# Kernel optimization log

Measured on AMD Instinct MI355X. Metric: run time of the kernel, lower is better.

Reference implementation:

```python
import jax, jax.numpy as jnp
import numpy as np

C, N, E, G = 8, 50000, 800000, 64
HID, HL, OL = 128, 2, 2
EPS = 1e-5


def sh_l012(vec):
    """e3nn real spherical harmonics l=0,1,2, normalize=True, component normalization. [E,3]->[E,9]"""
    r = jnp.sqrt(jnp.sum(vec * vec, axis=-1, keepdims=True) + 1e-12)
    u = vec / r
    x, y, z = u[:, 0], u[:, 1], u[:, 2]
    s3, s15, s5 = jnp.sqrt(3.0), jnp.sqrt(15.0), jnp.sqrt(5.0)
    y0 = jnp.ones_like(x)[:, None]
    y1 = s3 * u
    y2 = jnp.stack([s15 * x * z, s15 * x * y, s5 * (y * y - 0.5 * (x * x + z * z)),
                    s15 * y * z, 0.5 * s15 * (z * z - x * x)], axis=-1)
    return jnp.concatenate([y0, y1, y2], axis=-1)


def norm_act(s, v, d):
    """e3nn NormActivation(relu, eps): x * relu(n)/n per irrep instance."""
    ns = jnp.sqrt(s * s + EPS * EPS)
    nv = jnp.sqrt(jnp.sum(v * v, -1, keepdims=True) + EPS * EPS)
    nd = jnp.sqrt(jnp.sum(d * d, -1, keepdims=True) + EPS * EPS)
    return s * (jax.nn.relu(ns) / ns), v * (jax.nn.relu(nv) / nv), d * (jax.nn.relu(nd) / nd)


def o3_linear(s, v, d, W0, W1, W2):
    """o3.Linear: mixes multiplicities per l independently."""
    return s @ W0, jnp.einsum('nim,ic->ncm', v, W1), jnp.einsum('nim,ic->ncm', d, W2)


def tf_update(s, v, d, W0, W1, W2, Wd, edge_src, edge_dst):
    """Equivariant transformer update. W0/W1/W2 stacked [3(q,k,v), Cin, C], Wd [3(l), C, C]."""
    qs, qv, qd = norm_act(*o3_linear(s, v, d, W0[0], W1[0], W2[0]))
    ks, kv, kd = norm_act(*o3_linear(s, v, d, W0[1], W1[1], W2[1]))
    vs, vv, vd = norm_act(*o3_linear(s, v, d, W0[2], W1[2], W2[2]))
    # FullyConnectedTensorProduct(q,k)->0e: per-l channel-pair weighted inner products
    logit = (jnp.einsum('ec,ed,cd->e', qs[edge_dst], ks[edge_src], Wd[0])
             + jnp.einsum('ecm,edm,cd->e', qv[edge_dst], kv[edge_src], Wd[1]) / jnp.sqrt(3.0)
             + jnp.einsum('ecm,edm,cd->e', qd[edge_dst], kd[edge_src], Wd[2]) / jnp.sqrt(5.0))
    expv = jnp.exp(logit)
    z = jax.ops.segment_sum(expv, edge_dst, num_segments=N)
    z = jnp.where(z == 0, 1.0, z)
    w = jnp.sqrt(jax.nn.relu(expv / z[edge_dst]))  # relu(alpha).sqrt()
    os = jax.ops.segment_sum(w[:, None] * vs[edge_src], edge_dst, num_segments=N)
    ov = jax.ops.segment_sum(w[:, None, None] * vv[edge_src], edge_dst, num_segments=N)
    od = jax.ops.segment_sum(w[:, None, None] * vd[edge_src], edge_dst, num_segments=N)
    return os, ov, od


def setup_inputs() -> dict:
    key = jax.random.key(0)
    ks = jax.random.split(key, 20)
    inp = {}
    inp['x_scalars'] = jax.random.normal(ks[0], (N, 9), jnp.float32)
    inp['edge_vec'] = jax.random.normal(ks[1], (E, 3), jnp.float32)
    inp['et0_W0'] = jax.random.normal(ks[2], (3, 10, C), jnp.float32) / jnp.sqrt(10.0)
    inp['et0_W1'] = jax.random.normal(ks[3], (3, 1, C), jnp.float32)
    inp['et0_W2'] = jax.random.normal(ks[4], (3, 1, C), jnp.float32)
    inp['et0_Wd'] = jax.random.normal(ks[5], (3, C, C), jnp.float32) / C
    inp['h_W0'] = jax.random.normal(ks[6], (HL, 3, C, C), jnp.float32) / jnp.sqrt(float(C))
    inp['h_W1'] = jax.random.normal(ks[7], (HL, 3, C, C), jnp.float32) / jnp.sqrt(float(C))
    inp['h_W2'] = jax.random.normal(ks[8], (HL, 3, C, C), jnp.float32) / jnp.sqrt(float(C))
    inp['h_Wd'] = jax.random.normal(ks[9], (HL, 3, C, C), jnp.float32) / C
    inp['Wol'] = jax.random.normal(ks[10], (C, HID), jnp.float32) / jnp.sqrt(float(C))
    inp['Wlin'] = jax.random.normal(ks[11], (OL, HID, HID), jnp.float32) / jnp.sqrt(float(HID))
    inp['blin'] = jax.random.normal(ks[12], (OL, HID), jnp.float32) * 0.01
    inp['Wout'] = jax.random.normal(ks[13], (HID, 9), jnp.float32) / jnp.sqrt(float(HID))
    inp['bout'] = jax.random.normal(ks[14], (9,), jnp.float32) * 0.01
    inp['edge_src'] = jax.random.randint(ks[15], (E,), 0, N, jnp.int32)
    inp['edge_dst'] = jax.random.randint(ks[16], (E,), 0, N, jnp.int32)
    inp['batch_seg'] = jnp.sort(jax.random.randint(ks[17], (N,), 0, G, jnp.int32))
    return inp


def reference(x_scalars, edge_vec, et0_W0, et0_W1, et0_W2, et0_Wd,
              h_W0, h_W1, h_W2, h_Wd, Wol, Wlin, blin, Wout, bout,
              edge_src, edge_dst, batch_seg):
    sh = sh_l012(edge_vec)  # [E,9]
    cnt = jnp.maximum(jax.ops.segment_sum(jnp.ones((E,), sh.dtype), edge_dst, num_segments=N), 1.0)
    node_sh = jax.ops.segment_sum(sh, edge_dst, num_segments=N) / cnt[:, None]  # [N,9]
    s = jnp.concatenate([x_scalars, node_sh[:, :1]], axis=1)  # [N,10] 0e
    v = node_sh[:, 1:4][:, None, :]   # [N,1,3] 1e
    d = node_sh[:, 4:9][:, None, :]   # [N,1,5] 2e
    s, v, d = tf_update(s, v, d, et0_W0, et0_W1, et0_W2, et0_Wd, edge_src, edge_dst)
    for l in range(HL):
        hs, hv, hd = tf_update(s, v, d, h_W0[l], h_W1[l], h_W2[l], h_Wd[l], edge_src, edge_dst)
        s, v, d = s + hs, v + hv, d + hd
    # ol: irreps_output -> hidden x 0e (only scalar part maps to scalars)
    h = s @ Wol
    h = h / jnp.maximum(jnp.sqrt(jnp.sum(h * h, 1, keepdims=True)), 1e-12)  # F.normalize
    h = jax.nn.relu(h)
    for i in range(OL):
        h = jax.nn.relu(h @ Wlin[i] + blin[i])
    seg = batch_seg[edge_src]
    cg = jnp.maximum(jax.ops.segment_sum(jnp.ones((E,), h.dtype), seg, num_segments=G), 1.0)
    m = jax.ops.segment_sum(h[edge_src], seg, num_segments=G) / cg[:, None]
    return jax.nn.softmax(m @ Wout + bout, axis=1)
```

## Files before the change

kernel.cpp:

```cpp
#include <hip/hip_runtime.h>
#include <hip/hip_fp16.h>
#include <math.h>

#define NN 50000
#define NE 800000
#define NG 64
#define QH 80
#define KVH 144

__global__ void k_count(const int* __restrict__ esrc, const int* __restrict__ edst,
                        int* __restrict__ indeg_p, int* __restrict__ outdeg_p, int E)
{
  int e = blockIdx.x*blockDim.x + threadIdx.x;
  if (e >= E) return;
  int c = (e & 3) * NN;
  atomicAdd(indeg_p + c + edst[e], 1);
  atomicAdd(outdeg_p + c + esrc[e], 1);
}

__global__ void __launch_bounds__(256) k_scan1(const int* __restrict__ indeg_p,
                                               int* __restrict__ bsum, int N)
{
  __shared__ int sh[256];
  int t = threadIdx.x;
  int lo = blockIdx.x*2048 + t*8;
  int s = 0;
  #pragma unroll
  for (int k = 0; k < 8; ++k) {
    int i = lo + k;
    if (i < N)
      s += indeg_p[i] + indeg_p[NN+i] + indeg_p[2*NN+i] + indeg_p[3*NN+i];
  }
  sh[t] = s;
  __syncthreads();
  for (int off = 128; off > 0; off >>= 1) {
    if (t < off) sh[t] += sh[t+off];
    __syncthreads();
  }
  if (t == 0) bsum[blockIdx.x] = sh[0];
}

__global__ void k_scan2(int* __restrict__ bsum, int nb)
{
  if (threadIdx.x == 0) {
    int run = 0;
    for (int i = 0; i < nb; ++i) { int x = bsum[i]; bsum[i] = run; run += x; }
  }
}

__global__ void __launch_bounds__(256) k_scan3(const int* __restrict__ indeg_p,
                                               const int* __restrict__ outdeg_p,
                                               const int* __restrict__ bsum,
                                               int* __restrict__ rowptr,
                                               int* __restrict__ copybase,
                                               int* __restrict__ outdeg, int N)
{
  __shared__ int sh[256];
  int t = threadIdx.x;
  int lo = blockIdx.x*2048 + t*8;
  int tot[8];
  int s = 0;
  #pragma unroll
  for (int k = 0; k < 8; ++k) {
    int i = lo + k;
    int v = 0;
    if (i < N)
      v = indeg_p[i] + indeg_p[NN+i] + indeg_p[2*NN+i] + indeg_p[3*NN+i];
    tot[k] = v;
    s += v;
  }
  sh[t] = s;
  __syncthreads();
  for (int off = 1; off < 256; off <<= 1) {
    int x = 0;
    if (t >= off) x = sh[t-off];
    __syncthreads();
    if (t >= off) sh[t] += x;
    __syncthreads();
  }
  int run = bsum[blockIdx.x] + (t > 0 ? sh[t-1] : 0);
  #pragma unroll
  for (int k = 0; k < 8; ++k) {
    int i = lo + k;
    if (i < N) {
      int a0 = indeg_p[i], a1 = indeg_p[NN+i], a2 = indeg_p[2*NN+i];
      rowptr[i] = run;
      copybase[i]        = run;
      copybase[NN+i]     = run + a0;
      copybase[2*NN+i]   = run + a0 + a1;
      copybase[3*NN+i]   = run + a0 + a1 + a2;
      outdeg[i] = outdeg_p[i] + outdeg_p[NN+i] + outdeg_p[2*NN+i] + outdeg_p[3*NN+i];
    }
    if (i == N-1) rowptr[N] = run + tot[k];
    run += tot[k];
  }
}

__global__ void k_fill(const int* __restrict__ esrc, const int* __restrict__ edst,
                       const int* __restrict__ copybase, int* __restrict__ cursor_p,
                       int2* __restrict__ csr, int E)
{
  int e = blockIdx.x*blockDim.x + threadIdx.x;
  if (e >= E) return;
  int d = edst[e];
  int c = (e & 3) * NN;
  int slot = copybase[c + d] + atomicAdd(cursor_p + c + d, 1);
  csr[slot] = make_int2(esrc[e], e);
}

template<int CS, int CV, bool INIT>
__global__ void __launch_bounds__(256) k_node_feats(
    const float* __restrict__ in,
    const float* __restrict__ evec,
    const int2* __restrict__ csr,
    const int* __restrict__ rowptr,
    const float* __restrict__ W0,
    const float* __restrict__ W1,
    const float* __restrict__ W2,
    const float* __restrict__ Wd,
    __half* __restrict__ qt,
    __half* __restrict__ kv,
    int N)
{
  int n = blockIdx.x*blockDim.x + threadIdx.x;
  if (n >= N) return;
  float s_in[CS];
  float v_in[CV][3];
  float d_in[CV][5];

  if constexpr (INIT) {
    int b = rowptr[n], e2 = rowptr[n+1];
    float acc[9];
    #pragma unroll
    for (int j = 0; j < 9; ++j) acc[j] = 0.f;
    const float s3  = 1.7320508075688772f;
    const float s15 = 3.872983346207417f;
    const float s5  = 2.23606797749979f;
    for (int s = b; s < e2; ++s) {
      int eid = csr[s].y;
      float vx = evec[3*eid+0], vy = evec[3*eid+1], vz = evec[3*eid+2];
      float r = sqrtf(vx*vx + vy*vy + vz*vz + 1e-12f);
      float x = vx / r, y = vy / r, z = vz / r;
      acc[0] += 1.f;
      acc[1] += s3*x; acc[2] += s3*y; acc[3] += s3*z;
      acc[4] += s15*x*z;
      acc[5] += s15*x*y;
      acc[6] += s5*(y*y - 0.5f*(x*x + z*z));
      acc[7] += s15*y*z;
      acc[8] += 0.5f*s15*(z*z - x*x);
    }
    int dg = e2 - b;
    float inv = 1.f / (float)(dg > 1 ? dg : 1);
    #pragma unroll
    for (int j = 0; j < 9; ++j) s_in[j] = in[(size_t)n*9 + j];
    s_in[9] = acc[0]*inv;
    #pragma unroll
    for (int m = 0; m < 3; ++m) v_in[0][m] = acc[1+m]*inv;
    #pragma unroll
    for (int m = 0; m < 5; ++m) d_in[0][m] = acc[4+m]*inv;
  } else {
    float xf[72];
    const float4* xr = (const float4*)(in + (size_t)n*72);
    #pragma unroll
    for (int k = 0; k < 18; ++k) *(float4*)&xf[k*4] = xr[k];
    #pragma unroll
    for (int i = 0; i < CS; ++i) s_in[i] = xf[i];
    #pragma unroll
    for (int i = 0; i < CV; ++i)
      #pragma unroll
      for (int m = 0; m < 3; ++m) v_in[i][m] = xf[CS + i*3 + m];
    #pragma unroll
    for (int i = 0; i < CV; ++i)
      #pragma unroll
      for (int m = 0; m < 5; ++m) d_in[i][m] = xf[CS + 3*CV + i*5 + m];
  }

  const float inv_s3 = 0.5773502691896258f;
  const float inv_s5 = 0.4472135954999579f;

  #pragma unroll
  for (int t = 0; t < 3; ++t) {
    float ss[8];
    float vv[8][3];
    float dd[8][5];
    #pragma unroll
    for (int c = 0; c < 8; ++c) {
      float a = 0.f;
      #pragma unroll
      for (int i = 0; i < CS; ++i) a += s_in[i]*W0[t*CS*8 + i*8 + c];
      ss[c] = a;
    }
    #pragma unroll
    for (int c = 0; c < 8; ++c)
      #pragma unroll
      for (int m = 0; m < 3; ++m) {
        float a = 0.f;
        #pragma unroll
        for (int i = 0; i < CV; ++i) a += v_in[i][m]*W1[t*CV*8 + i*8 + c];
        vv[c][m] = a;
      }
    #pragma unroll
    for (int c = 0; c < 8; ++c)
      #pragma unroll
      for (int m = 0; m < 5; ++m) {
        float a = 0.f;
        #pragma unroll
        for (int i = 0; i < CV; ++i) a += d_in[i][m]*W2[t*CV*8 + i*8 + c];
        dd[c][m] = a;
      }

    if (t == 0) {
      __half* q = qt + (size_t)n*QH;
      #pragma unroll
      for (int dp = 0; dp < 8; ++dp) {
        float a = 0.f;
        #pragma unroll
        for (int c = 0; c < 8; ++c) a += ss[c]*Wd[0*64 + c*8 + dp];
        q[dp] = __float2half(a);
      }
      #pragma unroll
      for (int dp = 0; dp < 8; ++dp)
        #pragma unroll
        for (int m = 0; m < 3; ++m) {
          float a = 0.f;
          #pragma unroll
          for (int c = 0; c < 8; ++c) a += vv[c][m]*Wd[1*64 + c*8 + dp];
          q[8 + dp*3 + m] = __float2half(a*inv_s3);
        }
      #pragma unroll
      for (int dp = 0; dp < 8; ++dp)
        #pragma unroll
        for (int m = 0; m < 5; ++m) {
          float a = 0.f;
          #pragma unroll
          for (int c = 0; c < 8; ++c) a += dd[c][m]*Wd[2*64 + c*8 + dp];
          q[32 + dp*5 + m] = __float2half(a*inv_s5);
        }
    } else {
      __half* o = kv + (size_t)n*KVH + (t == 1 ? 0 : 72);
      #pragma unroll
      for (int c = 0; c < 8; ++c) o[c] = __float2half(ss[c]);
      #pragma unroll
      for (int c = 0; c < 8; ++c)
        #pragma unroll
        for (int m = 0; m < 3; ++m) o[8 + c*3 + m] = __float2half(vv[c][m]);
      #pragma unroll
      for (int c = 0; c < 8; ++c)
        #pragma unroll
        for (int m = 0; m < 5; ++m) o[32 + c*5 + m] = __float2half(dd[c][m]);
    }
  }
}

#define AT2_NPB 8
__global__ void __launch_bounds__(256) k_attn2(
    const __half* __restrict__ qt,
    const __half* __restrict__ kv,
    const int2* __restrict__ csr,
    const int* __restrict__ rowptr,
    const float* __restrict__ base,
    float* __restrict__ out, int N)
{
  typedef _Float16 h2 __attribute__((ext_vector_type(2)));
  const float LOG2E_HALF = 0.7213475204444817f;

  int t = threadIdx.x;
  int hw = t >> 5, lane = t & 31;
  int n = blockIdx.x*AT2_NPB + hw;
  if (n >= N) return;

  uint4 qraw = make_uint4(0,0,0,0);
  if (lane < 9)
    qraw = *(const uint4*)((const char*)qt + (size_t)n*(QH*2) + (size_t)lane*16);
  h2 qh0 = __builtin_bit_cast(h2, qraw.x);
  h2 qh1 = __builtin_bit_cast(h2, qraw.y);
  h2 qh2 = __builtin_bit_cast(h2, qraw.z);
  h2 qh3 = __builtin_bit_cast(h2, qraw.w);

  int b = rowptr[n], e2 = rowptr[n+1];
  float Z = 0.f;
  float A[8];
  #pragma unroll
  for (int i = 0; i < 8; ++i) A[i] = 0.f;

  const char* kvb = (const char*)kv;

  auto dot8 = [&](uint4 raw) -> float {
    float d = 0.f;
#if __has_builtin(__builtin_amdgcn_fdot2)
    d = __builtin_amdgcn_fdot2(qh0, __builtin_bit_cast(h2, raw.x), d, false);
    d = __builtin_amdgcn_fdot2(qh1, __builtin_bit_cast(h2, raw.y), d, false);
    d = __builtin_amdgcn_fdot2(qh2, __builtin_bit_cast(h2, raw.z), d, false);
    d = __builtin_amdgcn_fdot2(qh3, __builtin_bit_cast(h2, raw.w), d, false);
#else
    const __half* qp = (const __half*)&qraw;
    const __half* kp = (const __half*)&raw;
    #pragma unroll
    for (int i = 0; i < 8; ++i)
      d += __half2float(qp[i]) * __half2float(kp[i]);
#endif
    return d;
  };

  int s = b;
  for (; s + 4 <= e2; s += 4) {
    uint4 raw0 = make_uint4(0,0,0,0), raw1 = raw0, raw2 = raw0, raw3 = raw0;
    int src0 = csr[s].x, src1 = csr[s+1].x, src2 = csr[s+2].x, src3 = csr[s+3].x;
    if (lane < 18) {
      raw0 = *(const uint4*)(kvb + (size_t)src0*(KVH*2) + (size_t)lane*16);
      raw1 = *(const uint4*)(kvb + (size_t)src1*(KVH*2) + (size_t)lane*16);
      raw2 = *(const uint4*)(kvb + (size_t)src2*(KVH*2) + (size_t)lane*16);
      raw3 = *(const uint4*)(kvb + (size_t)src3*(KVH*2) + (size_t)lane*16);
    }
    float d0 = dot8(raw0), d1 = dot8(raw1), d2 = dot8(raw2), d3 = dot8(raw3);
    #pragma unroll
    for (int off = 1; off < 32; off <<= 1) {
      d0 += __shfl_xor(d0, off, 32);
      d1 += __shfl_xor(d1, off, 32);
      d2 += __shfl_xor(d2, off, 32);
      d3 += __shfl_xor(d3, off, 32);
    }
    float e0 = exp2f(LOG2E_HALF*d0);
    float e1 = exp2f(LOG2E_HALF*d1);
    float e2v = exp2f(LOG2E_HALF*d2);
    float e3 = exp2f(LOG2E_HALF*d3);
    Z += e0*e0 + e1*e1 + e2v*e2v + e3*e3;
    const __half* h0 = (const __half*)&raw0;
    const __half* h1 = (const __half*)&raw1;
    const __half* h2p = (const __half*)&raw2;
    const __half* h3 = (const __half*)&raw3;
    #pragma unroll
    for (int i = 0; i < 8; ++i)
      A[i] += e0*__half2float(h0[i]) + e1*__half2float(h1[i])
            + e2v*__half2float(h2p[i]) + e3*__half2float(h3[i]);
  }
  for (; s < e2; ++s) {
    uint4 raw0 = make_uint4(0,0,0,0);
    int src0 = csr[s].x;
    if (lane < 18)
      raw0 = *(const uint4*)(kvb + (size_t)src0*(KVH*2) + (size_t)lane*16);
    float d0 = dot8(raw0);
    #pragma unroll
    for (int off = 1; off < 32; off <<= 1) d0 += __shfl_xor(d0, off, 32);
    float e0 = exp2f(LOG2E_HALF*d0);
    Z += e0*e0;
    const __half* h0 = (const __half*)&raw0;
    #pragma unroll
    for (int i = 0; i < 8; ++i) A[i] += e0*__half2float(h0[i]);
  }

  float rz = (Z > 0.f) ? rsqrtf(Z) : 0.f;
  if (lane >= 9 && lane < 18) {
    int o0 = (lane - 9)*8;
    float r[8];
    #pragma unroll
    for (int i = 0; i < 8; ++i) r[i] = A[i]*rz;
    float* op = out + (size_t)n*72 + o0;
    if (base) {
      const float* bp = base + (size_t)n*72 + o0;
      #pragma unroll
      for (int i = 0; i < 8; ++i) r[i] += bp[i];
    }
    *(float4*)op     = make_float4(r[0], r[1], r[2], r[3]);
    *(float4*)(op+4) = make_float4(r[4], r[5], r[6], r[7]);
  }
}

#define HD_NODES 32
__global__ void __launch_bounds__(256) k_head(
    const float* __restrict__ svd,
    const float* __restrict__ Wol,
    const float* __restrict__ Wlin,
    const float* __restrict__ blin,
    const int* __restrict__ outdeg,
    const int* __restrict__ bseg,
    float* __restrict__ m,
    float* __restrict__ cg,
    int N)
{
  __shared__ float hs[HD_NODES][128];
  __shared__ float Ws[16][128];
  __shared__ float ssm[HD_NODES][8];
  int t = threadIdx.x;
  int n0 = blockIdx.x*HD_NODES;
  int tc = t & 31, tr = t >> 5;
  int c0 = tc*4;
  int nb = tr*4;

  {
    int node = t >> 3, i = t & 7;
    int gn = n0 + node;
    ssm[node][i] = (gn < N) ? svd[(size_t)gn*72 + i] : 0.f;
  }
  __syncthreads();

  float acc[4][4];
  #pragma unroll
  for (int nd = 0; nd < 4; ++nd)
    #pragma unroll
    for (int cc = 0; cc < 4; ++cc) acc[nd][cc] = 0.f;
  #pragma unroll
  for (int i = 0; i < 8; ++i) {
    float4 wv = *(const float4*)(Wol + i*128 + c0);
    #pragma unroll
    for (int nd = 0; nd < 4; ++nd) {
      float a = ssm[nb+nd][i];
      acc[nd][0] += a*wv.x; acc[nd][1] += a*wv.y;
      acc[nd][2] += a*wv.z; acc[nd][3] += a*wv.w;
    }
  }
  #pragma unroll
  for (int nd = 0; nd < 4; ++nd) {
    float p = acc[nd][0]*acc[nd][0] + acc[nd][1]*acc[nd][1]
            + acc[nd][2]*acc[nd][2] + acc[nd][3]*acc[nd][3];
    #pragma unroll
    for (int off = 1; off < 32; off <<= 1) p += __shfl_xor(p, off, 32);
    float rinv = 1.f / fmaxf(sqrtf(p), 1e-12f);
    *(float4*)&hs[nb+nd][c0] = make_float4(
        fmaxf(acc[nd][0]*rinv, 0.f), fmaxf(acc[nd][1]*rinv, 0.f),
        fmaxf(acc[nd][2]*rinv, 0.f), fmaxf(acc[nd][3]*rinv, 0.f));
  }

  for (int l = 0; l < 2; ++l) {
    float4 bv = *(const float4*)(blin + l*128 + c0);
    float a2[4][4];
    #pragma unroll
    for (int nd = 0; nd < 4; ++nd) {
      a2[nd][0]=bv.x; a2[nd][1]=bv.y; a2[nd][2]=bv.z; a2[nd][3]=bv.w;
    }
    #pragma unroll
    for (int q = 0; q < 8; ++q) {
      __syncthreads();
      {
        const float4* src = (const float4*)(Wlin + l*16384 + q*2048);
        float4* dst = (float4*)&Ws[0][0];
        dst[t] = src[t];
        dst[t + 256] = src[t + 256];
      }
      __syncthreads();
      int r0 = q*16;
      for (int i = 0; i < 16; i += 4) {
        float av[4][4];
        #pragma unroll
        for (int nd = 0; nd < 4; ++nd)
          *(float4*)av[nd] = *(const float4*)&hs[nb+nd][r0 + i];
        #pragma unroll
        for (int ii = 0; ii < 4; ++ii) {
          float4 wv = *(const float4*)&Ws[i+ii][c0];
          #pragma unroll
          for (int nd = 0; nd < 4; ++nd) {
            a2[nd][0] += av[nd][ii]*wv.x;
            a2[nd][1] += av[nd][ii]*wv.y;
            a2[nd][2] += av[nd][ii]*wv.z;
            a2[nd][3] += av[nd][ii]*wv.w;
          }
        }
      }
    }
    __syncthreads();
    #pragma unroll
    for (int nd = 0; nd < 4; ++nd)
      *(float4*)&hs[nb+nd][c0] = make_float4(
          fmaxf(a2[nd][0],0.f), fmaxf(a2[nd][1],0.f),
          fmaxf(a2[nd][2],0.f), fmaxf(a2[nd][3],0.f));
  }
  __syncthreads();

  if (t < 128) {
    int c = t;
    float accm = 0.f; int gprev = -1;
    for (int nn = 0; nn < HD_NODES; ++nn) {
      int n = n0 + nn;
      if (n >= N) break;
      int g = bseg[n];
      if (g != gprev) {
        if (gprev >= 0) atomicAdd(&m[gprev*128 + c], accm);
        accm = 0.f; gprev = g;
      }
      accm += (float)outdeg[n]*hs[nn][c];
    }
    if (gprev >= 0) atomicAdd(&m[gprev*128 + c], accm);
  } else if (t == 128) {
    float a = 0.f; int gp = -1;
    for (int nn = 0; nn < HD_NODES; ++nn) {
      int n = n0 + nn;
      if (n >= N) break;
      int g = bseg[n];
      if (g != gp) {
        if (gp >= 0) atomicAdd(&cg[gp], a);
        a = 0.f; gp = g;
      }
      a += (float)outdeg[n];
    }
    if (gp >= 0) atomicAdd(&cg[gp], a);
  }
}

__global__ void k_out(const float* __restrict__ m, const float* __restrict__ cg,
                      const float* __restrict__ Wout, const float* __restrict__ bout,
                      float* __restrict__ out)
{
  int g = threadIdx.x;
  if (g >= NG) return;
  float inv = 1.f / fmaxf(cg[g], 1.f);
  float v[9];
  #pragma unroll
  for (int j = 0; j < 9; ++j) {
    float a = 0.f;
    for (int i = 0; i < 128; ++i) a += m[g*128 + i]*Wout[i*9 + j];
    v[j] = a*inv + bout[j];
  }
  float mxv = v[0];
  #pragma unroll
  for (int j = 1; j < 9; ++j) mxv = fmaxf(mxv, v[j]);
  float sum = 0.f;
  #pragma unroll
  for (int j = 0; j < 9; ++j) { v[j] = expf(v[j] - mxv); sum += v[j]; }
  #pragma unroll
  for (int j = 0; j < 9; ++j) out[g*9 + j] = v[j]/sum;
}

extern "C" void kernel_launch(void* const* d_in, const int* in_sizes, int n_in,
                              void* d_out, int out_size, void* d_ws, size_t ws_size,
                              hipStream_t stream) {
  (void)in_sizes; (void)n_in; (void)out_size; (void)ws_size;
  const float* x_scalars = (const float*)d_in[0];
  const float* edge_vec  = (const float*)d_in[1];
  const float* et0_W0    = (const float*)d_in[2];
  const float* et0_W1    = (const float*)d_in[3];
  const float* et0_W2    = (const float*)d_in[4];
  const float* et0_Wd    = (const float*)d_in[5];
  const float* h_W0      = (const float*)d_in[6];
  const float* h_W1      = (const float*)d_in[7];
  const float* h_W2      = (const float*)d_in[8];
  const float* h_Wd      = (const float*)d_in[9];
  const float* Wol       = (const float*)d_in[10];
  const float* Wlin      = (const float*)d_in[11];
  const float* blin      = (const float*)d_in[12];
  const float* Wout      = (const float*)d_in[13];
  const float* bout      = (const float*)d_in[14];
  const int*   esrc      = (const int*)d_in[15];
  const int*   edst      = (const int*)d_in[16];
  const int*   bseg      = (const int*)d_in[17];

  const int N = NN, E = NE;

  char* w = (char*)d_ws;
  auto alloc = [&](size_t nbytes) {
    char* p = w;
    w += (nbytes + 255) & ~(size_t)255;
    return p;
  };
  int*    priv     = (int*)   alloc((size_t)12*N*4);
  int*    indeg_p  = priv;
  int*    outdeg_p = priv + 4*N;
  int*    cursor_p = priv + 8*N;
  int*    copybase = (int*)   alloc((size_t)4*N*4);
  int*    outdeg   = (int*)   alloc((size_t)N*4);
  int*    rowptr   = (int*)   alloc((size_t)(N+1)*4);
  int*    bsum     = (int*)   alloc((size_t)32*4);
  int2*   csr      = (int2*)  alloc((size_t)E*8);
  float*  stA      = (float*) alloc((size_t)N*72*4);
  float*  stB      = (float*) alloc((size_t)N*72*4);
  __half* qt       = (__half*)alloc((size_t)N*QH*2);
  __half* kv       = (__half*)alloc((size_t)N*KVH*2);
  float*  pool     = (float*) alloc((size_t)(NG*128 + NG)*4);
  float*  mpool    = pool;
  float*  cgp      = pool + NG*128;

  hipMemsetAsync(priv, 0, (size_t)12*N*4, stream);
  hipMemsetAsync(pool, 0, (size_t)(NG*128 + NG)*4, stream);

  const int TB = 256;
  const int gE  = (E + TB - 1) / TB;
  const int gN  = (N + TB - 1) / TB;
  const int gA2 = (N + AT2_NPB - 1) / AT2_NPB;
  const int gHD = (N + HD_NODES - 1) / HD_NODES;
  const int gSC = (N + 2047) / 2048;

  k_count<<<gE, TB, 0, stream>>>(esrc, edst, indeg_p, outdeg_p, E);
  k_scan1<<<gSC, 256, 0, stream>>>(indeg_p, bsum, N);
  k_scan2<<<1, 64, 0, stream>>>(bsum, gSC);
  k_scan3<<<gSC, 256, 0, stream>>>(indeg_p, outdeg_p, bsum, rowptr, copybase, outdeg, N);
  k_fill<<<gE, TB, 0, stream>>>(esrc, edst, copybase, cursor_p, csr, E);

  k_node_feats<10,1,true><<<gN, TB, 0, stream>>>(
      x_scalars, edge_vec, csr, rowptr,
      et0_W0, et0_W1, et0_W2, et0_Wd, qt, kv, N);
  k_attn2<<<gA2, 256, 0, stream>>>(qt, kv, csr, rowptr, nullptr, stA, N);

  float* cur = stA; float* oth = stB;
  for (int l = 0; l < 2; ++l) {
    k_node_feats<8,8,false><<<gN, TB, 0, stream>>>(
        cur, nullptr, nullptr, nullptr,
        h_W0 + l*192, h_W1 + l*192, h_W2 + l*192, h_Wd + l*192, qt, kv, N);
    k_attn2<<<gA2, 256, 0, stream>>>(qt, kv, csr, rowptr, cur, oth, N);
    float* t = cur; cur = oth; oth = t;
  }

  k_head<<<gHD, 256, 0, stream>>>(cur, Wol, Wlin, blin, outdeg, bseg, mpool, cgp, N);
  k_out<<<1, 64, 0, stream>>>(mpool, cgp, Wout, bout, (float*)d_out);
}
```

Baseline: 446.7 us.

## Use fp16 dot2 in head MLP and atomically bump copybase in CSR fill

The head kernel now stores hidden activations and weight tiles in shared memory as packed half2 and accumulates with the fdot2 builtin, which halves LDS traffic and FMA count for the two 128x128 layers. The CSR fill kernel increments copybase directly with atomicAdd instead of using a separate cursor array, which removes one gather and shrinks the memset. The fp16 rounding of activations and weights adds precision loss in the MLP head.

After: 446.3 us. Within noise of the previous version (-0.1%).

```diff
diff --git a/kernel.cpp b/kernel.cpp
--- a/kernel.cpp
+++ b/kernel.cpp
@@ -97,14 +97,13 @@
 }
 
 __global__ void k_fill(const int* __restrict__ esrc, const int* __restrict__ edst,
-                       const int* __restrict__ copybase, int* __restrict__ cursor_p,
-                       int2* __restrict__ csr, int E)
+                       int* __restrict__ copybase, int2* __restrict__ csr, int E)
 {
   int e = blockIdx.x*blockDim.x + threadIdx.x;
   if (e >= E) return;
   int d = edst[e];
   int c = (e & 3) * NN;
-  int slot = copybase[c + d] + atomicAdd(cursor_p + c + d, 1);
+  int slot = atomicAdd(copybase + c + d, 1);
   csr[slot] = make_int2(esrc[e], e);
 }
 
@@ -378,9 +377,10 @@
     float* __restrict__ cg,
     int N)
 {
-  __shared__ float hs[HD_NODES][128];
-  __shared__ float Ws[16][128];
-  __shared__ float ssm[HD_NODES][8];
+  typedef _Float16 h2 __attribute__((ext_vector_type(2)));
+  __shared__ __half2 hs2[HD_NODES][64];
+  __shared__ __half2 Wh2[8][128];
+  __shared__ float   ssm[HD_NODES][8];
   int t = threadIdx.x;
   int n0 = blockIdx.x*HD_NODES;
   int tc = t & 31, tr = t >> 5;
@@ -416,9 +416,10 @@
     #pragma unroll
     for (int off = 1; off < 32; off <<= 1) p += __shfl_xor(p, off, 32);
     float rinv = 1.f / fmaxf(sqrtf(p), 1e-12f);
-    *(float4*)&hs[nb+nd][c0] = make_float4(
-        fmaxf(acc[nd][0]*rinv, 0.f), fmaxf(acc[nd][1]*rinv, 0.f),
-        fmaxf(acc[nd][2]*rinv, 0.f), fmaxf(acc[nd][3]*rinv, 0.f));
+    float h0 = fmaxf(acc[nd][0]*rinv, 0.f), h1 = fmaxf(acc[nd][1]*rinv, 0.f);
+    float h2f = fmaxf(acc[nd][2]*rinv, 0.f), h3 = fmaxf(acc[nd][3]*rinv, 0.f);
+    hs2[nb+nd][tc*2]   = __floats2half2_rn(h0, h1);
+    hs2[nb+nd][tc*2+1] = __floats2half2_rn(h2f, h3);
   }
 
   for (int l = 0; l < 2; ++l) {
@@ -432,37 +433,68 @@
     for (int q = 0; q < 8; ++q) {
       __syncthreads();
       {
-        const float4* src = (const float4*)(Wlin + l*16384 + q*2048);
-        float4* dst = (float4*)&Ws[0][0];
-        dst[t] = src[t];
-        dst[t + 256] = src[t + 256];
+        #pragma unroll
+        for (int k = 0; k < 4; ++k) {
+          int idx = t + k*256;
+          int i2 = idx >> 7, c = idx & 127;
+          int r = q*16 + 2*i2;
+          float w0 = Wlin[l*16384 + r*128 + c];
+          float w1 = Wlin[l*16384 + (r+1)*128 + c];
+          Wh2[i2][c] = __floats2half2_rn(w0, w1);
+        }
       }
       __syncthreads();
-      int r0 = q*16;
-      for (int i = 0; i < 16; i += 4) {
-        float av[4][4];
-        #pragma unroll
-        for (int nd = 0; nd < 4; ++nd)
-          *(float4*)av[nd] = *(const float4*)&hs[nb+nd][r0 + i];
-        #pragma unroll
-        for (int ii = 0; ii < 4; ++ii) {
-          float4 wv = *(const float4*)&Ws[i+ii][c0];
+      uint4 ha[4], hb[4];
+      #pragma unroll
+      for (int nd = 0; nd < 4; ++nd) {
+        const uint4* hp = (const uint4*)&hs2[nb+nd][q*8];
+        ha[nd] = hp[0]; hb[nd] = hp[1];
+      }
+      #pragma unroll
+      for (int i2 = 0; i2 < 8; ++i2) {
+        uint4 wq = *(const uint4*)&Wh2[i2][c0];
+        unsigned hbits[4];
+        #pragma unroll
+        for (int nd = 0; nd < 4; ++nd) {
+          unsigned u;
+          if (i2 == 0) u = ha[nd].x; else if (i2 == 1) u = ha[nd].y;
+          else if (i2 == 2) u = ha[nd].z; else if (i2 == 3) u = ha[nd].w;
+          else if (i2 == 4) u = hb[nd].x; else if (i2 == 5) u = hb[nd].y;
+          else if (i2 == 6) u = hb[nd].z; else u = hb[nd].w;
+          hbits[nd] = u;
+        }
+#if __has_builtin(__builtin_amdgcn_fdot2)
+        #pragma unroll
+        for (int nd = 0; nd < 4; ++nd) {
+          h2 hh = __builtin_bit_cast(h2, hbits[nd]);
+          a2[nd][0] = __builtin_amdgcn_fdot2(hh, __builtin_bit_cast(h2, wq.x), a2[nd][0], false);
+          a2[nd][1] = __builtin_amdgcn_fdot2(hh, __builtin_bit_cast(h2, wq.y), a2[nd][1], false);
+          a2[nd][2] = __builtin_amdgcn_fdot2(hh, __builtin_bit_cast(h2, wq.z), a2[nd][2], false);
+          a2[nd][3] = __builtin_amdgcn_fdot2(hh, __builtin_bit_cast(h2, wq.w), a2[nd][3], false);
+        }
+#else
+        const __half2* wp = (const __half2*)&wq;
+        #pragma unroll
+        for (int nd = 0; nd < 4; ++nd) {
+          __half2 hh = __builtin_bit_cast(__half2, hbits[nd]);
+          float2 hf = __half22float2(hh);
           #pragma unroll
-          for (int nd = 0; nd < 4; ++nd) {
-            a2[nd][0] += av[nd][ii]*wv.x;
-            a2[nd][1] += av[nd][ii]*wv.y;
-            a2[nd][2] += av[nd][ii]*wv.z;
-            a2[nd][3] += av[nd][ii]*wv.w;
+          for (int cc = 0; cc < 4; ++cc) {
+            float2 wf = __half22float2(wp[cc]);
+            a2[nd][cc] += hf.x*wf.x + hf.y*wf.y;
           }
         }
+#endif
       }
     }
     __syncthreads();
     #pragma unroll
-    for (int nd = 0; nd < 4; ++nd)
-      *(float4*)&hs[nb+nd][c0] = make_float4(
-          fmaxf(a2[nd][0],0.f), fmaxf(a2[nd][1],0.f),
-          fmaxf(a2[nd][2],0.f), fmaxf(a2[nd][3],0.f));
+    for (int nd = 0; nd < 4; ++nd) {
+      float h0 = fmaxf(a2[nd][0],0.f), h1 = fmaxf(a2[nd][1],0.f);
+      float h2f = fmaxf(a2[nd][2],0.f), h3 = fmaxf(a2[nd][3],0.f);
+      hs2[nb+nd][tc*2]   = __floats2half2_rn(h0, h1);
+      hs2[nb+nd][tc*2+1] = __floats2half2_rn(h2f, h3);
+    }
   }
   __syncthreads();
 
@@ -477,7 +509,8 @@
         if (gprev >= 0) atomicAdd(&m[gprev*128 + c], accm);
         accm = 0.f; gprev = g;
       }
-      accm += (float)outdeg[n]*hs[nn][c];
+      float hv = __half2float(((const __half*)&hs2[nn][0])[c]);
+      accm += (float)outdeg[n]*hv;
     }
     if (gprev >= 0) atomicAdd(&m[gprev*128 + c], accm);
   } else if (t == 128) {
@@ -551,10 +584,9 @@
     w += (nbytes + 255) & ~(size_t)255;
     return p;
   };
-  int*    priv     = (int*)   alloc((size_t)12*N*4);
+  int*    priv     = (int*)   alloc((size_t)8*N*4);
   int*    indeg_p  = priv;
   int*    outdeg_p = priv + 4*N;
-  int*    cursor_p = priv + 8*N;
   int*    copybase = (int*)   alloc((size_t)4*N*4);
   int*    outdeg   = (int*)   alloc((size_t)N*4);
   int*    rowptr   = (int*)   alloc((size_t)(N+1)*4);
@@ -568,7 +600,7 @@
   float*  mpool    = pool;
   float*  cgp      = pool + NG*128;
 
-  hipMemsetAsync(priv, 0, (size_t)12*N*4, stream);
+  hipMemsetAsync(priv, 0, (size_t)8*N*4, stream);
   hipMemsetAsync(pool, 0, (size_t)(NG*128 + NG)*4, stream);
 
   const int TB = 256;
@@ -582,7 +614,7 @@
   k_scan1<<<gSC, 256, 0, stream>>>(indeg_p, bsum, N);
   k_scan2<<<1, 64, 0, stream>>>(bsum, gSC);
   k_scan3<<<gSC, 256, 0, stream>>>(indeg_p, outdeg_p, bsum, rowptr, copybase, outdeg, N);
-  k_fill<<<gE, TB, 0, stream>>>(esrc, edst, copybase, cursor_p, csr, E);
+  k_fill<<<gE, TB, 0, stream>>>(esrc, edst, copybase, csr, E);
 
   k_node_feats<10,1,true><<<gN, TB, 0, stream>>>(
       x_scalars, edge_vec, csr, rowptr,
```
